# Performance work log

Hardware: AMD Instinct MI355X
Metric: run time of the kernel (lower is better)

The kernel has to match this reference:

```python
import jax, jax.numpy as jnp
import numpy as np

B, N, C_IN, D, K = 4, 512, 256, 256, 20


def setup_inputs() -> dict:
    key = jax.random.key(0)
    ks = jax.random.split(key, 6)
    s_in = 1.0 / np.sqrt(C_IN)
    return {
        "x": jax.random.normal(ks[0], (B, N, C_IN), dtype=jnp.float32),
        "edge_index": jnp.zeros((2, 4), dtype=jnp.int64),
        "batch": jnp.zeros((B * N,), dtype=jnp.int64),
        "W_l": jax.random.uniform(ks[1], (D, C_IN), jnp.float32, -s_in, s_in),
        "b_l": jax.random.uniform(ks[2], (D,), jnp.float32, -s_in, s_in),
        "W_r": jax.random.uniform(ks[3], (D, C_IN), jnp.float32, -s_in, s_in),
        "b_r": jax.random.uniform(ks[4], (D,), jnp.float32, -s_in, s_in),
        "att": jax.random.normal(ks[5], (1, D), dtype=jnp.float32) * 0.1,
    }


def reference(x, edge_index, batch, W_l, b_l, W_r, b_r, att):
    b, n, _ = x.shape
    k = K
    # linear projections -> [b, n, d]
    x_l = jnp.einsum("bnc,dc->bnd", x, W_l) + b_l
    x_r = jnp.einsum("bnc,dc->bnd", x, W_r) + b_r
    # pairwise additive attention: [b, n, n, d]
    pair = x_l[:, :, None, :] + x_r[:, None, :, :]
    pair = jnp.where(pair >= 0, pair, 0.2 * pair)  # leaky_relu(0.2)
    alpha = jnp.einsum("bijd,d->bij", pair, att[0])  # [b, n, n]
    alpha = jnp.nan_to_num(alpha, nan=0.0, posinf=0.0, neginf=0.0)
    # knn reduction: topk over last dim
    attention, indices = jax.lax.top_k(alpha, k)  # [b, n, k]
    attention = jax.nn.softmax(attention, axis=-1).reshape(-1)  # [b*n*k]
    # edge index construction with per-batch node offsets
    offset = (jnp.arange(b, dtype=indices.dtype) * n)[:, None]  # [b, 1]
    index_i = jnp.repeat(jnp.arange(n, dtype=indices.dtype), k)[None, :] + offset
    index_j = indices.reshape(b, n * k) + offset
    new_edge_index = jnp.stack([index_i.reshape(-1), index_j.reshape(-1)], axis=0)
    # dropout is identity in eval mode; learn_sys=False -> return directly
    return new_edge_index, attention
```

## Files before the change

kernel.cpp:

```cpp
#include <hip/hip_runtime.h>
#include <math.h>


__global__ __launch_bounds__(256) void k_transpose(const float* __restrict__ Wl,
                                                   const float* __restrict__ Wr,
                                                   float* __restrict__ WtL,
                                                   float* __restrict__ WtR) {
    const int d = blockIdx.x, c = threadIdx.x;
    if (blockIdx.y == 0) WtL[c * 256 + d] = Wl[d * 256 + c];
    else                 WtR[c * 256 + d] = Wr[d * 256 + c];
}

__global__ __launch_bounds__(512, 4) void k_proj(const float* __restrict__ x,
        const float* __restrict__ WtL, const float* __restrict__ WtR,
        const float* __restrict__ bl, const float* __restrict__ br,
        const float* __restrict__ att,
        float* __restrict__ XL, float* __restrict__ XRt,
        float* __restrict__ Av, float* __restrict__ Bv) {
    __shared__ __align__(16) float xst[256 * 12];
    __shared__ __align__(16) float mrg[3 * 4096];
    const int tid = threadIdx.x;
    const int dq = tid & 63;
    const int rq = (tid >> 6) & 1;
    const int ch = tid >> 7;
    const int R = blockIdx.x * 8;
    const int b = R >> 9, jr0 = R & 511;

    {
        const float4 xv = ((const float4*)(x + (size_t)R * 256))[tid];
        const int r = tid >> 6;
        const int c4 = (tid & 63) * 4;
        xst[(c4 + 0) * 12 + r] = xv.x;
        xst[(c4 + 1) * 12 + r] = xv.y;
        xst[(c4 + 2) * 12 + r] = xv.z;
        xst[(c4 + 3) * 12 + r] = xv.w;
    }
    __syncthreads();

    float aL[4][4], aR[4][4];
#pragma unroll
    for (int r = 0; r < 4; ++r)
#pragma unroll
        for (int k = 0; k < 4; ++k) { aL[r][k] = 0.f; aR[r][k] = 0.f; }

    const int c0 = ch * 64;
    const float* WLp = WtL + (size_t)c0 * 256 + dq * 4;
    const float* WRp = WtR + (size_t)c0 * 256 + dq * 4;
#pragma unroll 4
    for (int cc = 0; cc < 64; ++cc) {
        const float4 wl = *(const float4*)(WLp + (size_t)cc * 256);
        const float4 wr = *(const float4*)(WRp + (size_t)cc * 256);
        const float4 xv = *(const float4*)&xst[(c0 + cc) * 12 + rq * 4];
#define PROJ_R(r, XS)                                  \
        aL[r][0] = fmaf(XS, wl.x, aL[r][0]);           \
        aL[r][1] = fmaf(XS, wl.y, aL[r][1]);           \
        aL[r][2] = fmaf(XS, wl.z, aL[r][2]);           \
        aL[r][3] = fmaf(XS, wl.w, aL[r][3]);           \
        aR[r][0] = fmaf(XS, wr.x, aR[r][0]);           \
        aR[r][1] = fmaf(XS, wr.y, aR[r][1]);           \
        aR[r][2] = fmaf(XS, wr.z, aR[r][2]);           \
        aR[r][3] = fmaf(XS, wr.w, aR[r][3]);
        PROJ_R(0, xv.x)
        PROJ_R(1, xv.y)
        PROJ_R(2, xv.z)
        PROJ_R(3, xv.w)
#undef PROJ_R
    }

    if (ch > 0) {
        float* m = &mrg[(ch - 1) * 4096];
#pragma unroll
        for (int r = 0; r < 4; ++r) {
            const int r8 = rq * 4 + r;
            *(float4*)&m[(r8 * 2 + 0) * 256 + dq * 4] = make_float4(aL[r][0], aL[r][1], aL[r][2], aL[r][3]);
            *(float4*)&m[(r8 * 2 + 1) * 256 + dq * 4] = make_float4(aR[r][0], aR[r][1], aR[r][2], aR[r][3]);
        }
    }
    __syncthreads();

    if (ch == 0) {
        const float4 bl4 = *(const float4*)&bl[dq * 4];
        const float4 br4 = *(const float4*)&br[dq * 4];
        const float4 at4 = *(const float4*)&att[dq * 4];
        float pa[4], pb[4];
#pragma unroll
        for (int r = 0; r < 4; ++r) {
            const int r8 = rq * 4 + r;
            const float4 mL0 = *(const float4*)&mrg[(r8 * 2 + 0) * 256 + dq * 4];
            const float4 mL1 = *(const float4*)&mrg[4096 + (r8 * 2 + 0) * 256 + dq * 4];
            const float4 mL2 = *(const float4*)&mrg[8192 + (r8 * 2 + 0) * 256 + dq * 4];
            const float4 mR0 = *(const float4*)&mrg[(r8 * 2 + 1) * 256 + dq * 4];
            const float4 mR1 = *(const float4*)&mrg[4096 + (r8 * 2 + 1) * 256 + dq * 4];
            const float4 mR2 = *(const float4*)&mrg[8192 + (r8 * 2 + 1) * 256 + dq * 4];
            float4 sl, sr;
            sl.x = aL[r][0] + mL0.x + mL1.x + mL2.x + bl4.x;
            sl.y = aL[r][1] + mL0.y + mL1.y + mL2.y + bl4.y;
            sl.z = aL[r][2] + mL0.z + mL1.z + mL2.z + bl4.z;
            sl.w = aL[r][3] + mL0.w + mL1.w + mL2.w + bl4.w;
            sr.x = aR[r][0] + mR0.x + mR1.x + mR2.x + br4.x;
            sr.y = aR[r][1] + mR0.y + mR1.y + mR2.y + br4.y;
            sr.z = aR[r][2] + mR0.z + mR1.z + mR2.z + br4.z;
            sr.w = aR[r][3] + mR0.w + mR1.w + mR2.w + br4.w;
            *(float4*)&XL[(size_t)(R + r8) * 256 + dq * 4] = sl;
            const size_t xrb0 = ((size_t)(b * 256 + dq * 4)) * 512 + jr0 + r8;
            XRt[xrb0 + 0 * 512] = sr.x;
            XRt[xrb0 + 1 * 512] = sr.y;
            XRt[xrb0 + 2 * 512] = sr.z;
            XRt[xrb0 + 3 * 512] = sr.w;
            pa[r] = at4.x * sl.x + at4.y * sl.y + at4.z * sl.z + at4.w * sl.w;
            pb[r] = at4.x * sr.x + at4.y * sr.y + at4.z * sr.z + at4.w * sr.w;
        }
#pragma unroll
        for (int r = 0; r < 4; ++r) {
#pragma unroll
            for (int off = 32; off; off >>= 1) {
                pa[r] += __shfl_xor(pa[r], off);
                pb[r] += __shfl_xor(pb[r], off);
            }
        }
        if (dq == 0) {
#pragma unroll
            for (int r = 0; r < 4; ++r) {
                Av[R + rq * 4 + r] = pa[r];
                Bv[R + rq * 4 + r] = pb[r];
            }
        }
    }
}

__global__ __launch_bounds__(512, 2) void k_pair_topk(const float* __restrict__ XL,
        const float* __restrict__ XRt, const float* __restrict__ Av,
        const float* __restrict__ Bv, const float* __restrict__ att,
        float* __restrict__ out) {
    __shared__ __align__(16) float xls[8 * 256];
    __shared__ __align__(16) float atts[256];
    __shared__ __align__(16) float mrg[3 * 4096];
    __shared__ __align__(16) float alph[8 * 512];
    const int tid = threadIdx.x;
    const int jc = tid & 127;
    const int h = tid >> 7;
    const int g = blockIdx.x;
    const int R = g * 8, b = R >> 9;

    ((float4*)xls)[tid] = ((const float4*)(XL + (size_t)R * 256))[tid];
    if (tid < 64) ((float4*)atts)[tid] = ((const float4*)att)[tid];
    __syncthreads();

    const int dbase = h * 64;
    const float* __restrict__ xrp = XRt + (size_t)b * 131072 + (size_t)dbase * 512 + jc * 4;

    float acc[8][4];
#pragma unroll
    for (int i = 0; i < 8; ++i)
#pragma unroll
        for (int c = 0; c < 4; ++c) acc[i][c] = 0.f;

    float4 bufA[8], bufB[8];
#pragma unroll
    for (int dd = 0; dd < 8; ++dd) bufA[dd] = *(const float4*)(xrp + (size_t)dd * 512);

#pragma unroll
    for (int ch = 0; ch < 8; ++ch) {
        const float4* cur = (ch & 1) ? bufB : bufA;
        float4* nxt = (ch & 1) ? bufA : bufB;
        if (ch < 7) {
            const float* p = xrp + (size_t)(ch + 1) * 8 * 512;
#pragma unroll
            for (int dd = 0; dd < 8; ++dd) nxt[dd] = *(const float4*)(p + (size_t)dd * 512);
        }
        const int d0 = dbase + ch * 8;
        const float4 at0 = *(const float4*)&atts[d0];
        const float4 at1 = *(const float4*)&atts[d0 + 4];
#pragma unroll
        for (int i = 0; i < 8; ++i) {
            const float4 xa = *(const float4*)&xls[i * 256 + d0];
            const float4 xb = *(const float4*)&xls[i * 256 + d0 + 4];
#define PSTEP(XLC, ATC, XR4)                                       \
            acc[i][0] = fmaf(ATC, fabsf(XLC + XR4.x), acc[i][0]);   \
            acc[i][1] = fmaf(ATC, fabsf(XLC + XR4.y), acc[i][1]);   \
            acc[i][2] = fmaf(ATC, fabsf(XLC + XR4.z), acc[i][2]);   \
            acc[i][3] = fmaf(ATC, fabsf(XLC + XR4.w), acc[i][3]);
            PSTEP(xa.x, at0.x, cur[0])
            PSTEP(xa.y, at0.y, cur[1])
            PSTEP(xa.z, at0.z, cur[2])
            PSTEP(xa.w, at0.w, cur[3])
            PSTEP(xb.x, at1.x, cur[4])
            PSTEP(xb.y, at1.y, cur[5])
            PSTEP(xb.z, at1.z, cur[6])
            PSTEP(xb.w, at1.w, cur[7])
#undef PSTEP
        }
    }

    if (h) {
        float* m = &mrg[(h - 1) * 4096];
#pragma unroll
        for (int i = 0; i < 8; ++i)
            *(float4*)&m[i * 512 + jc * 4] = make_float4(acc[i][0], acc[i][1], acc[i][2], acc[i][3]);
    }
    __syncthreads();
    if (h == 0) {
        const float4 Bj = *(const float4*)&Bv[b * 512 + jc * 4];
#pragma unroll
        for (int i = 0; i < 8; ++i) {
            const float Ai = Av[R + i];
            const float4 m0 = *(const float4*)&mrg[i * 512 + jc * 4];
            const float4 m1 = *(const float4*)&mrg[4096 + i * 512 + jc * 4];
            const float4 m2 = *(const float4*)&mrg[8192 + i * 512 + jc * 4];
            float a0 = fmaf(0.4f, acc[i][0] + m0.x + m1.x + m2.x, 0.6f * (Ai + Bj.x));
            float a1 = fmaf(0.4f, acc[i][1] + m0.y + m1.y + m2.y, 0.6f * (Ai + Bj.y));
            float a2 = fmaf(0.4f, acc[i][2] + m0.z + m1.z + m2.z, 0.6f * (Ai + Bj.z));
            float a3 = fmaf(0.4f, acc[i][3] + m0.w + m1.w + m2.w, 0.6f * (Ai + Bj.w));
            if (!isfinite(a0)) a0 = 0.f;
            if (!isfinite(a1)) a1 = 0.f;
            if (!isfinite(a2)) a2 = 0.f;
            if (!isfinite(a3)) a3 = 0.f;
            *(float4*)&alph[i * 512 + jc * 4] = make_float4(a0, a1, a2, a3);
        }
    }
    __syncthreads();

    const int lane = tid & 63;
    const int i = tid >> 6;
    const float* ar = &alph[i * 512];
    const float4 u0 = *(const float4*)&ar[lane * 8];
    const float4 u1 = *(const float4*)&ar[lane * 8 + 4];
    float v[8] = {u0.x, u0.y, u0.z, u0.w, u1.x, u1.y, u1.z, u1.w};

    float myval = 0.f, mmax = 0.f;
    int myidx = 0;
    for (int sel = 0; sel < 20; ++sel) {
        float bv = v[0]; int bt = 0;
#pragma unroll
        for (int t = 1; t < 8; ++t) { if (v[t] > bv) { bv = v[t]; bt = t; } }
        int bj = lane * 8 + bt;
#pragma unroll
        for (int off = 32; off; off >>= 1) {
            const float ov = __shfl_xor(bv, off);
            const int   oj = __shfl_xor(bj, off);
            if (ov > bv || (ov == bv && oj < bj)) { bv = ov; bj = oj; }
        }
        if (sel == 0) mmax = bv;
        if (lane == sel) { myval = bv; myidx = bj; }
        if ((bj >> 3) == lane) {
            const int bt2 = bj & 7;
#pragma unroll
            for (int t = 0; t < 8; ++t) if (t == bt2) v[t] = -INFINITY;
        }
    }
    const float e = (lane < 20) ? expf(myval - mmax) : 0.f;
    float s = e;
#pragma unroll
    for (int off = 32; off; off >>= 1) s += __shfl_xor(s, off);
    if (lane < 20) {
        const int row = R + i;
        const int base = row * 20 + lane;
        out[base] = (float)row;
        out[40960 + base] = (float)(b * 512 + myidx);
        out[81920 + base] = e / s;
    }
}

extern "C" void kernel_launch(void* const* d_in, const int* in_sizes, int n_in,
                              void* d_out, int out_size, void* d_ws, size_t ws_size,
                              hipStream_t stream) {
    const float* x   = (const float*)d_in[0];
    const float* Wl  = (const float*)d_in[3];
    const float* bl  = (const float*)d_in[4];
    const float* Wr  = (const float*)d_in[5];
    const float* br  = (const float*)d_in[6];
    const float* att = (const float*)d_in[7];

    float* ws  = (float*)d_ws;
    float* WtL = ws;
    float* WtR = ws + 65536;
    float* XL  = ws + 1048576;
    float* XRt = ws + 1572864;
    float* Av  = ws + 2097152;
    float* Bv  = ws + 2099200;
    float* out = (float*)d_out;

    k_transpose<<<dim3(256, 2), dim3(256), 0, stream>>>(Wl, Wr, WtL, WtR);
    k_proj<<<dim3(256), dim3(512), 0, stream>>>(x, WtL, WtR, bl, br, att, XL, XRt, Av, Bv);
    k_pair_topk<<<dim3(256), dim3(512), 0, stream>>>(XL, XRt, Av, Bv, att, out);
}
```

Before: 116.7 us.

## Stage XR transpose through LDS and fuse alpha merge into top-k load

In the projection kernel, the transposed XR output is first staged in shared memory, so each thread writes a coalesced float4 row segment instead of four scattered scalar stores. In the pair/top-k kernel, all four partial accumulators go to shared memory and every thread sums its own alpha values directly in the top-k load, with a strided j layout. This removes the serial merge stage run by only a quarter of the threads, plus one barrier and the separate alpha buffer. The cost is an extra barrier and LDS pass in the projection kernel and more LDS reads per top-k thread.

```diff
diff --git a/kernel.cpp b/kernel.cpp
--- a/kernel.cpp
+++ b/kernel.cpp
@@ -19,6 +19,7 @@
         float* __restrict__ Av, float* __restrict__ Bv) {
     __shared__ __align__(16) float xst[256 * 12];
     __shared__ __align__(16) float mrg[3 * 4096];
+    __shared__ __align__(16) float srs[8 * 256];
     const int tid = threadIdx.x;
     const int dq = tid & 63;
     const int rq = (tid >> 6) & 1;
@@ -78,11 +79,11 @@
     }
     __syncthreads();
 
+    float pa[4], pb[4];
     if (ch == 0) {
         const float4 bl4 = *(const float4*)&bl[dq * 4];
         const float4 br4 = *(const float4*)&br[dq * 4];
         const float4 at4 = *(const float4*)&att[dq * 4];
-        float pa[4], pb[4];
 #pragma unroll
         for (int r = 0; r < 4; ++r) {
             const int r8 = rq * 4 + r;
@@ -102,14 +103,25 @@
             sr.z = aR[r][2] + mR0.z + mR1.z + mR2.z + br4.z;
             sr.w = aR[r][3] + mR0.w + mR1.w + mR2.w + br4.w;
             *(float4*)&XL[(size_t)(R + r8) * 256 + dq * 4] = sl;
-            const size_t xrb0 = ((size_t)(b * 256 + dq * 4)) * 512 + jr0 + r8;
-            XRt[xrb0 + 0 * 512] = sr.x;
-            XRt[xrb0 + 1 * 512] = sr.y;
-            XRt[xrb0 + 2 * 512] = sr.z;
-            XRt[xrb0 + 3 * 512] = sr.w;
+            *(float4*)&srs[r8 * 256 + dq * 4] = sr;
             pa[r] = at4.x * sl.x + at4.y * sl.y + at4.z * sl.z + at4.w * sl.w;
             pb[r] = at4.x * sr.x + at4.y * sr.y + at4.z * sr.z + at4.w * sr.w;
         }
+    }
+    __syncthreads();
+
+    {
+        const int d = tid >> 1;
+        const int half = tid & 1;
+        float4 o;
+        o.x = srs[(half * 4 + 0) * 256 + d];
+        o.y = srs[(half * 4 + 1) * 256 + d];
+        o.z = srs[(half * 4 + 2) * 256 + d];
+        o.w = srs[(half * 4 + 3) * 256 + d];
+        *(float4*)&XRt[((size_t)(b * 256 + d)) * 512 + jr0 + half * 4] = o;
+    }
+
+    if (ch == 0) {
 #pragma unroll
         for (int r = 0; r < 4; ++r) {
 #pragma unroll
@@ -134,8 +146,7 @@
         float* __restrict__ out) {
     __shared__ __align__(16) float xls[8 * 256];
     __shared__ __align__(16) float atts[256];
-    __shared__ __align__(16) float mrg[3 * 4096];
-    __shared__ __align__(16) float alph[8 * 512];
+    __shared__ __align__(16) float mrg[4 * 4096];
     const int tid = threadIdx.x;
     const int jc = tid & 127;
     const int h = tid >> 7;
@@ -192,40 +203,31 @@
         }
     }
 
-    if (h) {
-        float* m = &mrg[(h - 1) * 4096];
+    {
+        float* m = &mrg[h * 4096];
 #pragma unroll
         for (int i = 0; i < 8; ++i)
             *(float4*)&m[i * 512 + jc * 4] = make_float4(acc[i][0], acc[i][1], acc[i][2], acc[i][3]);
     }
     __syncthreads();
-    if (h == 0) {
-        const float4 Bj = *(const float4*)&Bv[b * 512 + jc * 4];
-#pragma unroll
-        for (int i = 0; i < 8; ++i) {
-            const float Ai = Av[R + i];
-            const float4 m0 = *(const float4*)&mrg[i * 512 + jc * 4];
-            const float4 m1 = *(const float4*)&mrg[4096 + i * 512 + jc * 4];
-            const float4 m2 = *(const float4*)&mrg[8192 + i * 512 + jc * 4];
-            float a0 = fmaf(0.4f, acc[i][0] + m0.x + m1.x + m2.x, 0.6f * (Ai + Bj.x));
-            float a1 = fmaf(0.4f, acc[i][1] + m0.y + m1.y + m2.y, 0.6f * (Ai + Bj.y));
-            float a2 = fmaf(0.4f, acc[i][2] + m0.z + m1.z + m2.z, 0.6f * (Ai + Bj.z));
-            float a3 = fmaf(0.4f, acc[i][3] + m0.w + m1.w + m2.w, 0.6f * (Ai + Bj.w));
-            if (!isfinite(a0)) a0 = 0.f;
-            if (!isfinite(a1)) a1 = 0.f;
-            if (!isfinite(a2)) a2 = 0.f;
-            if (!isfinite(a3)) a3 = 0.f;
-            *(float4*)&alph[i * 512 + jc * 4] = make_float4(a0, a1, a2, a3);
-        }
-    }
-    __syncthreads();
 
     const int lane = tid & 63;
     const int i = tid >> 6;
-    const float* ar = &alph[i * 512];
-    const float4 u0 = *(const float4*)&ar[lane * 8];
-    const float4 u1 = *(const float4*)&ar[lane * 8 + 4];
-    float v[8] = {u0.x, u0.y, u0.z, u0.w, u1.x, u1.y, u1.z, u1.w};
+    const float Ai = Av[R + i];
+    const float* __restrict__ bvp = Bv + b * 512;
+    const float* __restrict__ mr = &mrg[i * 512];
+    float v[8];
+#pragma unroll
+    for (int t = 0; t < 8; ++t) {
+        const int j = t * 64 + lane;
+        float s = mr[j];
+        s += mr[4096 + j];
+        s += mr[8192 + j];
+        s += mr[12288 + j];
+        float a = fmaf(0.4f, s, 0.6f * (Ai + bvp[j]));
+        if (!isfinite(a)) a = 0.f;
+        v[t] = a;
+    }
 
     float myval = 0.f, mmax = 0.f;
     int myidx = 0;
@@ -233,7 +235,7 @@
         float bv = v[0]; int bt = 0;
 #pragma unroll
         for (int t = 1; t < 8; ++t) { if (v[t] > bv) { bv = v[t]; bt = t; } }
-        int bj = lane * 8 + bt;
+        int bj = bt * 64 + lane;
 #pragma unroll
         for (int off = 32; off; off >>= 1) {
             const float ov = __shfl_xor(bv, off);
@@ -242,8 +244,8 @@
         }
         if (sel == 0) mmax = bv;
         if (lane == sel) { myval = bv; myidx = bj; }
-        if ((bj >> 3) == lane) {
-            const int bt2 = bj & 7;
+        if ((bj & 63) == lane) {
+            const int bt2 = bj >> 6;
 #pragma unroll
             for (int t = 0; t < 8; ++t) if (t == bt2) v[t] = -INFINITY;
         }
```

Result: no change. 115.4 us (median of 2 runs) (-1.1%).
